# Performance work log

Measured on AMD Instinct MI355X. Metric: run time of the kernel, lower is better.

The kernel has to match this reference:

```python
import jax, jax.numpy as jnp
import numpy as np

EPS = 1e-6


def setup_inputs() -> dict:
    key = jax.random.key(0)
    k1, k2, k3, k4 = jax.random.split(key, 4)
    N, H, D = 262144, 256, 64  # total tokens, pc_hidden, cross_att_dim
    return {
        "yhat_embedding": jax.random.normal(k1, (N, H), dtype=jnp.float32),
        "y_embedding": jax.random.normal(k2, (N, H), dtype=jnp.float32),
        "k": jax.random.normal(k3, (H, D), dtype=jnp.float32),
        "q": jax.random.normal(k4, (H, D), dtype=jnp.float32),
        "seg_len": 64,  # uniform scope length (ragged scopes regularized)
    }


def reference(yhat_embedding, y_embedding, k, q, seg_len):
    # Project once for all tokens, then batch the per-segment attention.
    N, H = y_embedding.shape
    D = k.shape[1]
    B = N // seg_len
    yk = (y_embedding @ k).reshape(B, seg_len, D)       # y @ k per segment
    yq = (yhat_embedding @ q).reshape(B, seg_len, D)    # (q.T @ yhat.T).T
    scale = 1.0 / np.sqrt(D).astype(np.float32)
    # M[b] = (1/sqrt(D)) * (y@k) @ (yhat@q).T : [B, L, L]
    M = scale * jnp.einsum("bld,bmd->blm", yk, yq)
    attn = jax.nn.softmax(M, axis=2) + EPS               # softmax over dim=1 of [L,L]
    W = attn / attn.sum(axis=1, keepdims=True)           # column-normalize (axis=0 per segment)
    return W  # [B, L, L] stack of per-scope cross matrices
```

## Files before the change

kernel.cpp:

```cpp
#include <hip/hip_runtime.h>
#include <hip/hip_bf16.h>


#define H  256
#define D  64
#define L  64
#define LP 68

typedef __attribute__((ext_vector_type(8))) short frag_b;
typedef __attribute__((ext_vector_type(4))) float frag_acc;

__device__ inline unsigned short f32_bf16_rne(float f) {
    unsigned u = __float_as_uint(f);
    u += 0x7FFFu + ((u >> 16) & 1u);
    return (unsigned short)(u >> 16);
}
__device__ inline float bf16_f32(unsigned short h) {
    return __uint_as_float(((unsigned)h) << 16);
}

__global__ void prep_kq(const float* __restrict__ k, const float* __restrict__ q,
                        unsigned short* __restrict__ planes) {
    int tid = blockIdx.x * 256 + threadIdx.x;
    const float* src = (tid < H * D) ? k : q;
    int base = (tid < H * D) ? 0 : 2 * H * D;
    int e = tid & (H * D - 1);
    int h = e >> 6, d = e & 63;
    float x = src[e];
    unsigned short hi = f32_bf16_rne(x);
    float rem = x - bf16_f32(hi);
    unsigned short lo = f32_bf16_rne(rem);
    int o = d * H + h;
    planes[base + o] = hi;
    planes[base + H * D + o] = lo;
}

__global__ __launch_bounds__(256) void cross_attn(
        const float* __restrict__ yhat, const float* __restrict__ y,
        const unsigned short* __restrict__ planes, float* __restrict__ out) {
    __shared__ __align__(16) float s_yk[L * LP];
    __shared__ __align__(16) float s_yq[L * LP];
    __shared__ __align__(16) float s_M[L * LP];
    __shared__ float s_cs[4 * L];

    const int b    = blockIdx.x;
    const int tid  = threadIdx.x;
    const int wave = tid >> 6;
    const int lane = tid & 63;
    const int ln   = lane & 15;
    const int kg   = lane >> 4;

    const bool isQ = (wave >= 2);
    const float* src = isQ ? yhat : y;
    const frag_b* bph = (const frag_b*)(planes + (isQ ? 2 * H * D : 0));
    const frag_b* bpl = bph + (H * D) / 8;
    const int rowbase = (wave & 1) * 32;

    const frag_acc zf = {0.f, 0.f, 0.f, 0.f};
    frag_acc acc[2][4];
    #pragma unroll
    for (int rt = 0; rt < 2; rt++)
        #pragma unroll
        for (int t = 0; t < 4; t++) acc[rt][t] = zf;

    const float* abase = src + ((size_t)b * L + rowbase + ln) * H + kg * 8;

    #pragma unroll 2
    for (int ks = 0; ks < 8; ks++) {
        const int kb = ks * 32;
        frag_b ah[2], al[2];
        #pragma unroll
        for (int rt = 0; rt < 2; rt++) {
            const float4* ap = (const float4*)(abase + (size_t)rt * 16 * H + kb);
            float4 v0 = ap[0], v1 = ap[1];
            float xs[8] = {v0.x, v0.y, v0.z, v0.w, v1.x, v1.y, v1.z, v1.w};
            #pragma unroll
            for (int j = 0; j < 8; j++) {
                unsigned short hb = f32_bf16_rne(xs[j]);
                ah[rt][j] = (short)hb;
                al[rt][j] = (short)f32_bf16_rne(xs[j] - bf16_f32(hb));
            }
        }
        #pragma unroll
        for (int t = 0; t < 4; t++) {
            int n = t * 16 + ln;
            frag_b bh = bph[n * (H / 8) + ks * 4 + kg];
            frag_b bl = bpl[n * (H / 8) + ks * 4 + kg];
            #pragma unroll
            for (int rt = 0; rt < 2; rt++) {
                acc[rt][t] = __builtin_amdgcn_mfma_f32_16x16x32_bf16(ah[rt], bh, acc[rt][t], 0, 0, 0);
                acc[rt][t] = __builtin_amdgcn_mfma_f32_16x16x32_bf16(ah[rt], bl, acc[rt][t], 0, 0, 0);
                acc[rt][t] = __builtin_amdgcn_mfma_f32_16x16x32_bf16(al[rt], bh, acc[rt][t], 0, 0, 0);
            }
        }
    }
    {
        float* dstP = isQ ? s_yq : s_yk;
        #pragma unroll
        for (int rt = 0; rt < 2; rt++)
            #pragma unroll
            for (int t = 0; t < 4; t++)
                #pragma unroll
                for (int i = 0; i < 4; i++)
                    dstP[(rowbase + rt * 16 + kg * 4 + i) * LP + t * 16 + ln] = acc[rt][t][i];
    }
    __syncthreads();

    frag_acc mac[4];
    #pragma unroll
    for (int t = 0; t < 4; t++) mac[t] = zf;

    #pragma unroll
    for (int dk = 0; dk < 2; dk++) {
        const int db = dk * 32;
        frag_b ah, al;
        {
            const float* ap = &s_yk[(wave * 16 + ln) * LP + db + kg * 8];
            #pragma unroll
            for (int j = 0; j < 8; j++) {
                float x = ap[j];
                unsigned short hb = f32_bf16_rne(x);
                ah[j] = (short)hb;
                al[j] = (short)f32_bf16_rne(x - bf16_f32(hb));
            }
        }
        #pragma unroll
        for (int t = 0; t < 4; t++) {
            frag_b bh, bl;
            const float* bp = &s_yq[(t * 16 + ln) * LP + db + kg * 8];
            #pragma unroll
            for (int j = 0; j < 8; j++) {
                float x = bp[j];
                unsigned short hb = f32_bf16_rne(x);
                bh[j] = (short)hb;
                bl[j] = (short)f32_bf16_rne(x - bf16_f32(hb));
            }
            mac[t] = __builtin_amdgcn_mfma_f32_16x16x32_bf16(ah, bh, mac[t], 0, 0, 0);
            mac[t] = __builtin_amdgcn_mfma_f32_16x16x32_bf16(ah, bl, mac[t], 0, 0, 0);
            mac[t] = __builtin_amdgcn_mfma_f32_16x16x32_bf16(al, bh, mac[t], 0, 0, 0);
        }
    }
    #pragma unroll
    for (int t = 0; t < 4; t++)
        #pragma unroll
        for (int i = 0; i < 4; i++)
            s_M[(wave * 16 + kg * 4 + i) * LP + t * 16 + ln] = 0.125f * mac[t][i];
    __syncthreads();

    float attn[16];
    float cs = 0.f;
    #pragma unroll
    for (int i = 0; i < 16; i++) {
        float v = s_M[(wave * 16 + i) * LP + lane];
        float mx = v;
        #pragma unroll
        for (int off = 32; off > 0; off >>= 1) mx = fmaxf(mx, __shfl_xor(mx, off, 64));
        float e = __expf(v - mx);
        float s = e;
        #pragma unroll
        for (int off = 32; off > 0; off >>= 1) s += __shfl_xor(s, off, 64);
        float a = e / s + 1e-6f;
        attn[i] = a;
        cs += a;
    }
    s_cs[wave * 64 + lane] = cs;
    __syncthreads();
    const float tot = s_cs[lane] + s_cs[64 + lane] + s_cs[128 + lane] + s_cs[192 + lane];
    const float inv = 1.f / tot;
    float* ob = out + (size_t)b * (L * L);
    #pragma unroll
    for (int i = 0; i < 16; i++)
        ob[(wave * 16 + i) * 64 + lane] = attn[i] * inv;
}

extern "C" void kernel_launch(void* const* d_in, const int* in_sizes, int n_in,
                              void* d_out, int out_size, void* d_ws, size_t ws_size,
                              hipStream_t stream) {
    const float* yhat = (const float*)d_in[0];
    const float* y    = (const float*)d_in[1];
    const float* k    = (const float*)d_in[2];
    const float* q    = (const float*)d_in[3];
    float* outp = (float*)d_out;
    unsigned short* planes = (unsigned short*)d_ws;

    const int N = in_sizes[0] / H;
    const int B = N / L;

    prep_kq<<<(2 * H * D) / 256, 256, 0, stream>>>(k, q, planes);
    cross_attn<<<B, 256, 0, stream>>>(yhat, y, planes, outp);
}
```

Measured before the change: 642.8 us.

## Store projections as swizzled bf16 hi/lo planes and softmax in MFMA registers

Projection results are split into bf16 hi/lo planes once and written to shared memory in an XOR-swizzled layout, so the second matmul loads fragments directly instead of re-splitting fp32 values per use. The softmax and column sums now run on the MFMA accumulator registers with 16-lane shuffles, which removes the s_M shared-memory round trip. Shared memory drops from about 52KB to 32KB, and launch bounds request 5 blocks per SM for more occupancy. Global loads are also hoisted ahead of the conversion work. Output stores now come out in the accumulator layout, which may coalesce less well.

```diff
diff --git a/kernel.cpp b/kernel.cpp
--- a/kernel.cpp
+++ b/kernel.cpp
@@ -1,11 +1,9 @@
 #include <hip/hip_runtime.h>
-#include <hip/hip_bf16.h>
 
 
 #define H  256
 #define D  64
 #define L  64
-#define LP 68
 
 typedef __attribute__((ext_vector_type(8))) short frag_b;
 typedef __attribute__((ext_vector_type(4))) float frag_acc;
@@ -17,6 +15,10 @@
 }
 __device__ inline float bf16_f32(unsigned short h) {
     return __uint_as_float(((unsigned)h) << 16);
+}
+
+__device__ inline int pswz(int row, int col) {
+    return (row << 6) + ((((col >> 3) ^ row) & 7) << 3) + (col & 7);
 }
 
 __global__ void prep_kq(const float* __restrict__ k, const float* __restrict__ q,
@@ -35,13 +37,10 @@
     planes[base + H * D + o] = lo;
 }
 
-__global__ __launch_bounds__(256) void cross_attn(
+__global__ __launch_bounds__(256, 5) void cross_attn(
         const float* __restrict__ yhat, const float* __restrict__ y,
         const unsigned short* __restrict__ planes, float* __restrict__ out) {
-    __shared__ __align__(16) float s_yk[L * LP];
-    __shared__ __align__(16) float s_yq[L * LP];
-    __shared__ __align__(16) float s_M[L * LP];
-    __shared__ float s_cs[4 * L];
+    __shared__ __align__(16) unsigned short s_pl[4 * L * D];
 
     const int b    = blockIdx.x;
     const int tid  = threadIdx.x;
@@ -68,12 +67,18 @@
     #pragma unroll 2
     for (int ks = 0; ks < 8; ks++) {
         const int kb = ks * 32;
-        frag_b ah[2], al[2];
+        float4 v[2][2];
         #pragma unroll
         for (int rt = 0; rt < 2; rt++) {
             const float4* ap = (const float4*)(abase + (size_t)rt * 16 * H + kb);
-            float4 v0 = ap[0], v1 = ap[1];
-            float xs[8] = {v0.x, v0.y, v0.z, v0.w, v1.x, v1.y, v1.z, v1.w};
+            v[rt][0] = ap[0];
+            v[rt][1] = ap[1];
+        }
+        frag_b ah[2], al[2];
+        #pragma unroll
+        for (int rt = 0; rt < 2; rt++) {
+            float xs[8] = {v[rt][0].x, v[rt][0].y, v[rt][0].z, v[rt][0].w,
+                           v[rt][1].x, v[rt][1].y, v[rt][1].z, v[rt][1].w};
             #pragma unroll
             for (int j = 0; j < 8; j++) {
                 unsigned short hb = f32_bf16_rne(xs[j]);
@@ -94,83 +99,91 @@
             }
         }
     }
+
     {
-        float* dstP = isQ ? s_yq : s_yk;
+        unsigned short* dstH = s_pl + (isQ ? 2 * L * D : 0);
+        unsigned short* dstL = dstH + L * D;
         #pragma unroll
         for (int rt = 0; rt < 2; rt++)
             #pragma unroll
             for (int t = 0; t < 4; t++)
                 #pragma unroll
-                for (int i = 0; i < 4; i++)
-                    dstP[(rowbase + rt * 16 + kg * 4 + i) * LP + t * 16 + ln] = acc[rt][t][i];
+                for (int i = 0; i < 4; i++) {
+                    int row = rowbase + rt * 16 + kg * 4 + i;
+                    int col = t * 16 + ln;
+                    float x = acc[rt][t][i];
+                    unsigned short hb = f32_bf16_rne(x);
+                    int o = pswz(row, col);
+                    dstH[o] = hb;
+                    dstL[o] = f32_bf16_rne(x - bf16_f32(hb));
+                }
     }
     __syncthreads();
 
+    const unsigned short* ykH = s_pl;
+    const unsigned short* ykL = s_pl + L * D;
+    const unsigned short* yqH = s_pl + 2 * L * D;
+    const unsigned short* yqL = s_pl + 3 * L * D;
+
     frag_acc mac[4];
     #pragma unroll
     for (int t = 0; t < 4; t++) mac[t] = zf;
 
     #pragma unroll
     for (int dk = 0; dk < 2; dk++) {
-        const int db = dk * 32;
-        frag_b ah, al;
-        {
-            const float* ap = &s_yk[(wave * 16 + ln) * LP + db + kg * 8];
-            #pragma unroll
-            for (int j = 0; j < 8; j++) {
-                float x = ap[j];
-                unsigned short hb = f32_bf16_rne(x);
-                ah[j] = (short)hb;
-                al[j] = (short)f32_bf16_rne(x - bf16_f32(hb));
-            }
-        }
+        const int colb = dk * 32 + kg * 8;
+        frag_b ah = *(const frag_b*)(ykH + pswz(wave * 16 + ln, colb));
+        frag_b al = *(const frag_b*)(ykL + pswz(wave * 16 + ln, colb));
         #pragma unroll
         for (int t = 0; t < 4; t++) {
-            frag_b bh, bl;
-            const float* bp = &s_yq[(t * 16 + ln) * LP + db + kg * 8];
-            #pragma unroll
-            for (int j = 0; j < 8; j++) {
-                float x = bp[j];
-                unsigned short hb = f32_bf16_rne(x);
-                bh[j] = (short)hb;
-                bl[j] = (short)f32_bf16_rne(x - bf16_f32(hb));
-            }
+            frag_b bh = *(const frag_b*)(yqH + pswz(t * 16 + ln, colb));
+            frag_b bl = *(const frag_b*)(yqL + pswz(t * 16 + ln, colb));
             mac[t] = __builtin_amdgcn_mfma_f32_16x16x32_bf16(ah, bh, mac[t], 0, 0, 0);
             mac[t] = __builtin_amdgcn_mfma_f32_16x16x32_bf16(ah, bl, mac[t], 0, 0, 0);
             mac[t] = __builtin_amdgcn_mfma_f32_16x16x32_bf16(al, bh, mac[t], 0, 0, 0);
         }
     }
-    #pragma unroll
-    for (int t = 0; t < 4; t++)
+    __syncthreads();
+
+    float* s_cs = (float*)s_pl;
+
+    float a[4][4];
+    float colpart[4] = {0.f, 0.f, 0.f, 0.f};
+    #pragma unroll
+    for (int i = 0; i < 4; i++) {
+        float v0 = 0.125f * mac[0][i], v1 = 0.125f * mac[1][i];
+        float v2 = 0.125f * mac[2][i], v3 = 0.125f * mac[3][i];
+        float mx = fmaxf(fmaxf(v0, v1), fmaxf(v2, v3));
+        #pragma unroll
+        for (int off = 8; off >= 1; off >>= 1) mx = fmaxf(mx, __shfl_xor(mx, off, 64));
+        float e0 = __expf(v0 - mx), e1 = __expf(v1 - mx);
+        float e2 = __expf(v2 - mx), e3 = __expf(v3 - mx);
+        float s = (e0 + e1) + (e2 + e3);
+        #pragma unroll
+        for (int off = 8; off >= 1; off >>= 1) s += __shfl_xor(s, off, 64);
+        float rs = 1.f / s;
+        a[0][i] = e0 * rs + 1e-6f; a[1][i] = e1 * rs + 1e-6f;
+        a[2][i] = e2 * rs + 1e-6f; a[3][i] = e3 * rs + 1e-6f;
+        colpart[0] += a[0][i]; colpart[1] += a[1][i];
+        colpart[2] += a[2][i]; colpart[3] += a[3][i];
+    }
+    #pragma unroll
+    for (int t = 0; t < 4; t++) {
+        colpart[t] += __shfl_xor(colpart[t], 16, 64);
+        colpart[t] += __shfl_xor(colpart[t], 32, 64);
+    }
+    s_cs[wave * 64 + kg * 16 + ln] = colpart[kg];
+    __syncthreads();
+
+    float* ob = out + (size_t)b * (L * L);
+    #pragma unroll
+    for (int t = 0; t < 4; t++) {
+        int c = t * 16 + ln;
+        float inv = 1.f / (s_cs[c] + s_cs[64 + c] + s_cs[128 + c] + s_cs[192 + c]);
         #pragma unroll
         for (int i = 0; i < 4; i++)
-            s_M[(wave * 16 + kg * 4 + i) * LP + t * 16 + ln] = 0.125f * mac[t][i];
-    __syncthreads();
-
-    float attn[16];
-    float cs = 0.f;
-    #pragma unroll
-    for (int i = 0; i < 16; i++) {
-        float v = s_M[(wave * 16 + i) * LP + lane];
-        float mx = v;
-        #pragma unroll
-        for (int off = 32; off > 0; off >>= 1) mx = fmaxf(mx, __shfl_xor(mx, off, 64));
-        float e = __expf(v - mx);
-        float s = e;
-        #pragma unroll
-        for (int off = 32; off > 0; off >>= 1) s += __shfl_xor(s, off, 64);
-        float a = e / s + 1e-6f;
-        attn[i] = a;
-        cs += a;
-    }
-    s_cs[wave * 64 + lane] = cs;
-    __syncthreads();
-    const float tot = s_cs[lane] + s_cs[64 + lane] + s_cs[128 + lane] + s_cs[192 + lane];
-    const float inv = 1.f / tot;
-    float* ob = out + (size_t)b * (L * L);
-    #pragma unroll
-    for (int i = 0; i < 16; i++)
-        ob[(wave * 16 + i) * 64 + lane] = attn[i] * inv;
+            ob[(wave * 16 + kg * 4 + i) * 64 + c] = a[t][i] * inv;
+    }
 }
 
 extern "C" void kernel_launch(void* const* d_in, const int* in_sizes, int n_in,
```

Result: faster. 604.0 us (-6.0%).
